# Kernel tuning notes

Hardware: AMD Instinct MI355X
Metric: run time of the kernel (lower is better)

The kernel has to match this reference:

```python
import jax, jax.numpy as jnp
import numpy as np

B, CIN, L = 4, 128, 2048
D_MODEL, D_STATE, EXPAND, HEADDIM, NGROUPS = 256, 16, 3, 3, 1
D_INNER = EXPAND * D_MODEL            # 768
NHEADS = D_INNER // HEADDIM           # 256
CONV_DIM = D_INNER + 2 * NGROUPS * D_STATE   # 800
D_IN_PROJ = 2 * D_INNER + 2 * NGROUPS * D_STATE + NHEADS  # 1824
K_PROJ, D_CONV = 4, 4
EPS = 1e-5


def setup_inputs() -> dict:
    key = jax.random.key(0)
    ks = jax.random.split(key, 9)
    x = jax.random.normal(ks[0], (B, CIN, L), jnp.float32)
    proj_w = jax.random.normal(ks[1], (D_MODEL, CIN, K_PROJ), jnp.float32) / np.float32(np.sqrt(CIN * K_PROJ))
    in_proj_w = jax.random.normal(ks[2], (D_IN_PROJ, D_MODEL), jnp.float32) / np.float32(np.sqrt(D_MODEL))
    conv_w = jax.random.normal(ks[3], (CONV_DIM, 1, D_CONV), jnp.float32) / np.float32(np.sqrt(D_CONV))
    conv_b = jax.random.normal(ks[4], (CONV_DIM,), jnp.float32) * 0.01
    # dt_bias = inverse-softplus of dt ~ LogUniform[1e-3, 1e-1] (mamba2 init)
    u = jax.random.uniform(ks[5], (NHEADS,), jnp.float32)
    dt = jnp.exp(u * np.float32(np.log(0.1) - np.log(1e-3)) + np.float32(np.log(1e-3)))
    dt_bias = dt + jnp.log(-jnp.expm1(-dt))
    A_log = jnp.log(1.0 + 15.0 * jax.random.uniform(ks[6], (NHEADS,), jnp.float32))  # A in [-16,-1]
    D_skip = jnp.ones((NHEADS,), jnp.float32)
    norm_w = jnp.ones((D_INNER,), jnp.float32)
    out_proj_w = jax.random.normal(ks[7], (D_MODEL, D_INNER), jnp.float32) / np.float32(np.sqrt(D_INNER))
    return {"x": x, "proj_w": proj_w, "in_proj_w": in_proj_w, "conv_w": conv_w,
            "conv_b": conv_b, "dt_bias": dt_bias, "A_log": A_log, "D_skip": D_skip,
            "norm_w": norm_w, "out_proj_w": out_proj_w}


def _forward(x, proj_w, in_proj_w, conv_w, conv_b, dt_bias, A_log, D_skip, norm_w, out_proj_w):
    # outer Conv1d, padding='same' (k=4 -> left 1, right 2), no bias: (B,CIN,L)->(B,D_MODEL,L)
    h = jax.lax.conv_general_dilated(x, proj_w, (1,), [(1, 2)],
                                     dimension_numbers=("NCH", "OIH", "NCH"))
    u = h.transpose(0, 2, 1)                          # (B, L, d_model)
    zxbcdt = jnp.einsum("bld,ed->ble", u, in_proj_w)  # (B, L, 1824)
    z = zxbcdt[..., :D_INNER]                                     # (B,L,768)
    xBC = zxbcdt[..., D_INNER:D_INNER + CONV_DIM]                 # (B,L,800)
    dt = zxbcdt[..., D_INNER + CONV_DIM:]                         # (B,L,256)
    dt = jax.nn.softplus(dt + dt_bias)
    # depthwise causal conv (pad d_conv-1 on left) + SiLU
    xBC_c = jax.lax.conv_general_dilated(xBC.transpose(0, 2, 1), conv_w, (1,), [(D_CONV - 1, 0)],
                                         feature_group_count=CONV_DIM,
                                         dimension_numbers=("NCH", "OIH", "NCH"))
    xBC = jax.nn.silu(xBC_c + conv_b[None, :, None]).transpose(0, 2, 1)  # (B,L,800)
    xs = xBC[..., :D_INNER].reshape(B, L, NHEADS, HEADDIM)        # (B,L,H,P)
    Bm = xBC[..., D_INNER:D_INNER + D_STATE]                      # (B,L,N) (ngroups=1)
    Cm = xBC[..., D_INNER + D_STATE:]                             # (B,L,N)
    A = -jnp.exp(A_log)                                           # (H,)

    def step(hst, inp):
        dt_t, x_t, B_t, C_t = inp                 # (B,H),(B,H,P),(B,N),(B,N)
        dA = jnp.exp(dt_t * A)[:, :, None, None]  # (B,H,1,1)
        hst = dA * hst + jnp.einsum("bh,bhp,bn->bhpn", dt_t, x_t, B_t)
        y_t = jnp.einsum("bhpn,bn->bhp", hst, C_t)
        return hst, y_t

    h0 = jnp.zeros((B, NHEADS, HEADDIM, D_STATE), x.dtype)
    _, ys = jax.lax.scan(step, h0, (dt.transpose(1, 0, 2), xs.transpose(1, 0, 2, 3),
                                    Bm.transpose(1, 0, 2), Cm.transpose(1, 0, 2)))
    y = ys.transpose(1, 0, 2, 3) + D_skip[None, None, :, None] * xs   # (B,L,H,P)
    y = y.reshape(B, L, D_INNER)
    # gated RMSNorm: gate first, then normalize (norm_before_gate=False)
    y = y * jax.nn.silu(z)
    y = y * jax.lax.rsqrt(jnp.mean(y * y, axis=-1, keepdims=True) + EPS) * norm_w
    out = jnp.einsum("ble,de->bld", y, out_proj_w)   # (B,L,d_model)
    return out.transpose(0, 2, 1)                    # (B,d_model,L)


def reference(x, proj_w, in_proj_w, conv_w, conv_b, dt_bias, A_log, D_skip, norm_w, out_proj_w):
    return _forward(x, proj_w, in_proj_w, conv_w, conv_b, dt_bias, A_log, D_skip, norm_w, out_proj_w)
```

## Files before the change

kernel.cpp:

```cpp
#include <hip/hip_runtime.h>
#include <hip/hip_fp16.h>
#include <math.h>

#define B_     4
#define CIN    128
#define LEN    2048
#define DMODEL 256
#define DSTATE 16
#define NHEADS 256
#define DINNER 768
#define CONVDIM 800
#define DINPROJ 1824
#define EPS_   1e-5f
#define CHUNK  64
#define NCHUNK 32

typedef _Float16 f16x8 __attribute__((ext_vector_type(8)));
typedef float    f32x4 __attribute__((ext_vector_type(4)));

__device__ __forceinline__ float silu_(float x){ return x / (1.0f + __expf(-x)); }
__device__ __forceinline__ float softplus_(float x){
    return x > 0.f ? x + log1pf(__expf(-x)) : log1pf(__expf(x));
}

__device__ __forceinline__ void gl2lds16(const _Float16* g, _Float16* l){
    __builtin_amdgcn_global_load_lds(
        (const __attribute__((address_space(1))) void*)g,
        (__attribute__((address_space(3))) void*)l, 16, 0, 0);
}

__global__ __launch_bounds__(256) void k_f2h(const float* __restrict__ a,
                                             _Float16* __restrict__ o, int n){
    for (int i = blockIdx.x * 256 + threadIdx.x; i < n; i += gridDim.x * 256)
        o[i] = (_Float16)a[i];
}

__global__ __launch_bounds__(256) void k_im2col(const float* __restrict__ x,
                                                _Float16* __restrict__ xcol){
    __shared__ float xs[CIN][68];
    int blk = blockIdx.x;
    int b  = blk >> 5;
    int l0 = (blk & 31) << 6;
    const float* xb = x + (size_t)b * CIN * LEN;
    for (int idx = threadIdx.x; idx < CIN * 67; idx += 256){
        int ci = idx / 67, j = idx % 67;
        int gl = l0 - 1 + j;
        xs[ci][j] = (gl >= 0 && gl < LEN) ? xb[ci * LEN + gl] : 0.f;
    }
    __syncthreads();
    #pragma unroll
    for (int v = 0; v < 16; v++){
        int id = v * 256 + threadIdx.x;
        int rl = id >> 6, c = id & 63;
        f16x8 pk;
        #pragma unroll
        for (int e = 0; e < 8; e++){
            int ci = c * 2 + (e >> 2), k = e & 3;
            pk[e] = (_Float16)xs[ci][rl + k];
        }
        *(f16x8*)&xcol[((size_t)(b * LEN + l0 + rl)) * 512 + c * 8] = pk;
    }
}

template<int K, int EPI>
__global__ __launch_bounds__(256) void k_gemm(const _Float16* __restrict__ A,
                                              const _Float16* __restrict__ Bw,
                                              const float* __restrict__ dt_bias,
                                              _Float16* __restrict__ o_u,
                                              _Float16* __restrict__ o_z,
                                              _Float16* __restrict__ o_xbc,
                                              _Float16* __restrict__ o_dt,
                                              float* __restrict__ o_f){
    __shared__ __align__(16) _Float16 As[128 * 32];
    __shared__ __align__(16) _Float16 Bs[128 * 32];
    int tid  = threadIdx.x;
    int wv   = tid >> 6;
    int lane = tid & 63;
    int quad = lane >> 4;
    int l16  = lane & 15;
    int m0 = blockIdx.x * 128;
    int n0 = blockIdx.y * 128;
    int wm = (wv >> 1) * 64;
    int wn = (wv & 1) * 64;
    int srow = lane >> 2;
    int scol = (lane & 3) * 8;

    f32x4 acc[4][4];
    #pragma unroll
    for (int i = 0; i < 4; i++)
        #pragma unroll
        for (int j = 0; j < 4; j++)
            acc[i][j] = (f32x4){0.f, 0.f, 0.f, 0.f};

    for (int k0 = 0; k0 < K; k0 += 32){
        #pragma unroll
        for (int j = 0; j < 2; j++){
            int ar = m0 + wv * 32 + j * 16 + srow;
            gl2lds16(A + (size_t)ar * K + k0 + scol,
                     &As[(wv * 32 + j * 16) * 32]);
            int nr = n0 + wv * 32 + j * 16 + srow;
            if (EPI == 1) nr = nr > (DINPROJ - 1) ? (DINPROJ - 1) : nr;
            gl2lds16(Bw + (size_t)nr * K + k0 + scol,
                     &Bs[(wv * 32 + j * 16) * 32]);
        }
        __syncthreads();
        f16x8 af[4], bf[4];
        #pragma unroll
        for (int i = 0; i < 4; i++)
            af[i] = *(const f16x8*)&As[(wm + i * 16 + l16) * 32 + quad * 8];
        #pragma unroll
        for (int j = 0; j < 4; j++)
            bf[j] = *(const f16x8*)&Bs[(wn + j * 16 + l16) * 32 + quad * 8];
        #pragma unroll
        for (int i = 0; i < 4; i++)
            #pragma unroll
            for (int j = 0; j < 4; j++)
                acc[i][j] = __builtin_amdgcn_mfma_f32_16x16x32_f16(
                                af[i], bf[j], acc[i][j], 0, 0, 0);
        __syncthreads();
    }

    if (EPI == 0){
        #pragma unroll
        for (int j = 0; j < 4; j++){
            int col = n0 + wn + j * 16 + l16;
            #pragma unroll
            for (int i = 0; i < 4; i++){
                int row = m0 + wm + i * 16 + quad * 4;
                #pragma unroll
                for (int r = 0; r < 4; r++)
                    o_u[(size_t)(row + r) * DMODEL + col] = (_Float16)acc[i][j][r];
            }
        }
    } else if (EPI == 1){
        #pragma unroll
        for (int j = 0; j < 4; j++){
            int col = n0 + wn + j * 16 + l16;
            if (col < DINNER){
                #pragma unroll
                for (int i = 0; i < 4; i++){
                    int row = m0 + wm + i * 16 + quad * 4;
                    #pragma unroll
                    for (int r = 0; r < 4; r++)
                        o_z[(size_t)(row + r) * DINNER + col] = (_Float16)acc[i][j][r];
                }
            } else if (col < DINNER + CONVDIM){
                int cc = col - DINNER;
                #pragma unroll
                for (int i = 0; i < 4; i++){
                    int row = m0 + wm + i * 16 + quad * 4;
                    #pragma unroll
                    for (int r = 0; r < 4; r++)
                        o_xbc[(size_t)(row + r) * CONVDIM + cc] = (_Float16)acc[i][j][r];
                }
            } else if (col < DINPROJ){
                int hh = col - (DINNER + CONVDIM);
                float bias = dt_bias[hh];
                #pragma unroll
                for (int i = 0; i < 4; i++){
                    int row = m0 + wm + i * 16 + quad * 4;
                    #pragma unroll
                    for (int r = 0; r < 4; r++)
                        o_dt[(size_t)(row + r) * NHEADS + hh] =
                            (_Float16)softplus_(acc[i][j][r] + bias);
                }
            }
        }
    } else {
        #pragma unroll
        for (int i = 0; i < 4; i++){
            int row = m0 + wm + i * 16 + quad * 4;
            int b = row >> 11, l = row & (LEN - 1);
            #pragma unroll
            for (int j = 0; j < 4; j++){
                int d = n0 + wn + j * 16 + l16;
                *(f32x4*)&o_f[(((size_t)(b * DMODEL + d)) << 11) + l] = acc[i][j];
            }
        }
    }
}

__global__ __launch_bounds__(256) void k_dwconv(const __half* __restrict__ xbc,
                                                const float* __restrict__ cw,
                                                const float* __restrict__ cb,
                                                __half* __restrict__ xcc){
    int idx = blockIdx.x * 256 + threadIdx.x;
    int c = idx % CONVDIM;
    int r = idx / CONVDIM;
    int l = r & (LEN - 1);
    float4 wv = *(const float4*)(cw + c * 4);
    float acc = cb[c];
    if (l >= 3){
        const __half* base = xbc + (size_t)(r - 3) * CONVDIM + c;
        acc += __half2float(base[0]) * wv.x + __half2float(base[CONVDIM]) * wv.y +
               __half2float(base[2 * CONVDIM]) * wv.z + __half2float(base[3 * CONVDIM]) * wv.w;
    } else {
        const float wk[4] = {wv.x, wv.y, wv.z, wv.w};
        for (int k = 0; k < 4; k++){
            int t = l - 3 + k;
            if (t >= 0) acc += __half2float(xbc[(size_t)(r + k - 3) * CONVDIM + c]) * wk[k];
        }
    }
    xcc[idx] = __float2half(silu_(acc));
}

__global__ __launch_bounds__(64) void k_scanA(const __half* __restrict__ dtb,
                                              const __half* __restrict__ xcc,
                                              const float* __restrict__ A_log,
                                              __half* __restrict__ cstate,
                                              float* __restrict__ dsum){
    int blk = blockIdx.x;
    int c  = blk & (NCHUNK - 1);
    int hg = (blk >> 5) & 63;
    int b  = blk >> 11;
    int lane = threadIdx.x;
    int hl = lane >> 4;
    int n  = lane & 15;
    int h  = hg * 4 + hl;
    int c0 = h * 3;
    float A = -__expf(A_log[h]);
    int t0 = c * CHUNK;
    const __half* xr  = xcc + ((size_t)b * LEN + t0) * CONVDIM;
    const __half* dtp = dtb + ((size_t)b * LEN + t0) * NHEADS + h;
    float h0 = 0.f, h1 = 0.f, h2 = 0.f, sdt = 0.f;
    for (int t = 0; t < CHUNK; t++){
        float vx0 = __half2float(xr[c0]);
        float vx1 = __half2float(xr[c0 + 1]);
        float vx2 = __half2float(xr[c0 + 2]);
        float vB  = __half2float(xr[DINNER + n]);
        float cdt = __half2float(dtp[(size_t)t * NHEADS]);
        float dA  = __expf(cdt * A);
        float dtB = cdt * vB;
        h0 = fmaf(h0, dA, vx0 * dtB);
        h1 = fmaf(h1, dA, vx1 * dtB);
        h2 = fmaf(h2, dA, vx2 * dtB);
        sdt += cdt;
        xr += CONVDIM;
    }
    size_t sbase = (((size_t)(b * NHEADS + h)) * NCHUNK + c) * 48;
    cstate[sbase + n]      = __float2half(h0);
    cstate[sbase + 16 + n] = __float2half(h1);
    cstate[sbase + 32 + n] = __float2half(h2);
    if (n == 0) dsum[(size_t)(b * NHEADS + h) * NCHUNK + c] = __expf(A * sdt);
}

__global__ __launch_bounds__(64) void k_scanB(__half* __restrict__ cstate,
                                              const float* __restrict__ dsum){
    int bh = blockIdx.x;
    int lane = threadIdx.x;
    if (lane >= 48) return;
    __half* st = cstate + (size_t)bh * NCHUNK * 48 + lane;
    const float* dd = dsum + (size_t)bh * NCHUNK;
    float H = 0.f;
    for (int c = 0; c < NCHUNK; c++){
        float d = dd[c];
        float s = __half2float(st[(size_t)c * 48]);
        st[(size_t)c * 48] = __float2half(H);
        H = fmaf(H, d, s);
    }
}

__global__ __launch_bounds__(64) void k_scanC(const __half* __restrict__ dtb,
                                              const __half* __restrict__ xcc,
                                              const float* __restrict__ A_log,
                                              const float* __restrict__ D_skip,
                                              const __half* __restrict__ cstate,
                                              __half* __restrict__ y){
    int blk = blockIdx.x;
    int c  = blk & (NCHUNK - 1);
    int hg = (blk >> 5) & 63;
    int b  = blk >> 11;
    int lane = threadIdx.x;
    int hl = lane >> 4;
    int n  = lane & 15;
    int h  = hg * 4 + hl;
    int c0 = h * 3;
    float A   = -__expf(A_log[h]);
    float Dsk = D_skip[h];
    int t0 = c * CHUNK;
    const __half* xr  = xcc + ((size_t)b * LEN + t0) * CONVDIM;
    const __half* dtp = dtb + ((size_t)b * LEN + t0) * NHEADS + h;
    size_t sbase = (((size_t)(b * NHEADS + h)) * NCHUNK + c) * 48;
    float h0 = __half2float(cstate[sbase + n]);
    float h1 = __half2float(cstate[sbase + 16 + n]);
    float h2 = __half2float(cstate[sbase + 32 + n]);
    __half* yp = y + ((size_t)b * LEN + t0) * DINNER + c0;
    for (int t = 0; t < CHUNK; t++){
        float vx0 = __half2float(xr[c0]);
        float vx1 = __half2float(xr[c0 + 1]);
        float vx2 = __half2float(xr[c0 + 2]);
        float vB  = __half2float(xr[DINNER + n]);
        float vC  = __half2float(xr[DINNER + DSTATE + n]);
        float cdt = __half2float(dtp[(size_t)t * NHEADS]);
        float dA  = __expf(cdt * A);
        float dtB = cdt * vB;
        h0 = fmaf(h0, dA, vx0 * dtB);
        h1 = fmaf(h1, dA, vx1 * dtB);
        h2 = fmaf(h2, dA, vx2 * dtB);
        float p0 = h0 * vC, p1 = h1 * vC, p2 = h2 * vC;
        #pragma unroll
        for (int m = 1; m < 16; m <<= 1){
            p0 += __shfl_xor(p0, m, 64);
            p1 += __shfl_xor(p1, m, 64);
            p2 += __shfl_xor(p2, m, 64);
        }
        if (n < 3){
            float pv = (n == 0) ? p0 : ((n == 1) ? p1 : p2);
            float xv = (n == 0) ? vx0 : ((n == 1) ? vx1 : vx2);
            yp[n] = __float2half(fmaf(Dsk, xv, pv));
        }
        xr += CONVDIM;
        yp += DINNER;
    }
}

__global__ __launch_bounds__(256) void k_norm(__half* __restrict__ y,
                                              const __half* __restrict__ z,
                                              const float* __restrict__ nw){
    __shared__ float wsum[4];
    size_t r = blockIdx.x;
    int tid = threadIdx.x;
    const __half* zr = z + r * DINNER;
    __half* yr = y + r * DINNER;
    int e0 = tid, e1 = tid + 256, e2 = tid + 512;
    float t0 = __half2float(yr[e0]) * silu_(__half2float(zr[e0]));
    float t1 = __half2float(yr[e1]) * silu_(__half2float(zr[e1]));
    float t2 = __half2float(yr[e2]) * silu_(__half2float(zr[e2]));
    float ss = t0 * t0 + t1 * t1 + t2 * t2;
    #pragma unroll
    for (int m = 1; m < 64; m <<= 1) ss += __shfl_xor(ss, m, 64);
    if ((tid & 63) == 0) wsum[tid >> 6] = ss;
    __syncthreads();
    float tot = wsum[0] + wsum[1] + wsum[2] + wsum[3];
    float sc = rsqrtf(tot / (float)DINNER + EPS_);
    yr[e0] = __float2half(t0 * sc * nw[e0]);
    yr[e1] = __float2half(t1 * sc * nw[e1]);
    yr[e2] = __float2half(t2 * sc * nw[e2]);
}

extern "C" void kernel_launch(void* const* d_in, const int* in_sizes, int n_in,
                              void* d_out, int out_size, void* d_ws, size_t ws_size,
                              hipStream_t stream) {
    const float* x          = (const float*)d_in[0];
    const float* proj_w     = (const float*)d_in[1];
    const float* in_proj_w  = (const float*)d_in[2];
    const float* conv_w     = (const float*)d_in[3];
    const float* conv_b     = (const float*)d_in[4];
    const float* dt_bias    = (const float*)d_in[5];
    const float* A_log      = (const float*)d_in[6];
    const float* D_skip     = (const float*)d_in[7];
    const float* norm_w     = (const float*)d_in[8];
    const float* out_proj_w = (const float*)d_in[9];
    float* out = (float*)d_out;

    char* ob = (char*)d_out;
    _Float16* pw_h  = (_Float16*)ob;
    _Float16* ipw_h = (_Float16*)(ob + 262144);

    char* wsb = (char*)d_ws;
    _Float16* xcol  = (_Float16*)(wsb);
    _Float16* u_h   = (_Float16*)(wsb + 8388608);
    __half*   xcc_h = (__half*)(wsb);
    __half*   z_h   = (__half*)(wsb + 13107200);
    __half*   xbc_h = (__half*)(wsb + 25690112);
    __half*   y_h   = xbc_h;
    __half*   dt_h  = (__half*)(wsb + 38797312);
    __half*   cstate= (__half*)(wsb + 42991616);
    float*    dsum  = (float*)(wsb + 46137344);
    _Float16* opw_h = (_Float16*)(wsb + 46268416);

    k_f2h   <<<64, 256, 0, stream>>>(proj_w,     pw_h,  DMODEL * CIN * 4);
    k_f2h   <<<64, 256, 0, stream>>>(in_proj_w,  ipw_h, DINPROJ * DMODEL);
    k_f2h   <<<64, 256, 0, stream>>>(out_proj_w, opw_h, DMODEL * DINNER);
    k_im2col<<<128, 256, 0, stream>>>(x, xcol);
    k_gemm<512, 0><<<dim3(64, 2), 256, 0, stream>>>(xcol, pw_h, nullptr,
        u_h, nullptr, nullptr, nullptr, nullptr);
    k_gemm<256, 1><<<dim3(64, 15), 256, 0, stream>>>(u_h, ipw_h, dt_bias,
        nullptr, (_Float16*)z_h, (_Float16*)xbc_h, (_Float16*)dt_h, nullptr);
    k_dwconv<<<25600, 256, 0, stream>>>(xbc_h, conv_w, conv_b, xcc_h);
    k_scanA <<<8192, 64, 0, stream>>>(dt_h, xcc_h, A_log, cstate, dsum);
    k_scanB <<<1024, 64, 0, stream>>>(cstate, dsum);
    k_scanC <<<8192, 64, 0, stream>>>(dt_h, xcc_h, A_log, D_skip, cstate, y_h);
    k_norm  <<<8192, 256, 0, stream>>>(y_h, z_h, norm_w);
    k_gemm<768, 2><<<dim3(64, 2), 256, 0, stream>>>((const _Float16*)y_h, opw_h,
        nullptr, nullptr, nullptr, nullptr, nullptr, out);
}
```

Baseline: 318.5 us.

## Restructure chunked scan: fuse intra-chunk pass, add parallel inter-chunk state fixup

The chunked selective scan used to make two sequential passes over every chunk: one pass produced the end-of-chunk states, then a second pass recomputed the recurrence from the carried-in state. Now a single pass computes the zero-initialised intra-chunk outputs and chunk states together. A new parallel fixup kernel then adds the carried state's contribution to y, using a prefix sum of dt for the decay and a dot product of C with the state. Separately, the three weight-conversion launches are merged into one kernel. The cost is an extra read-modify-write of y in fp16 plus a wave-level prefix scan, and fp16 rounding of the partial y may change accuracy slightly.

```diff
diff --git a/kernel.cpp b/kernel.cpp
--- a/kernel.cpp
+++ b/kernel.cpp
@@ -29,10 +29,19 @@
         (__attribute__((address_space(3))) void*)l, 16, 0, 0);
 }
 
-__global__ __launch_bounds__(256) void k_f2h(const float* __restrict__ a,
-                                             _Float16* __restrict__ o, int n){
-    for (int i = blockIdx.x * 256 + threadIdx.x; i < n; i += gridDim.x * 256)
-        o[i] = (_Float16)a[i];
+__global__ __launch_bounds__(256) void k_f2h3(const float* __restrict__ a0,
+                                              const float* __restrict__ a1,
+                                              const float* __restrict__ a2,
+                                              _Float16* __restrict__ o0,
+                                              _Float16* __restrict__ o1,
+                                              _Float16* __restrict__ o2,
+                                              int n0, int n1, int n2){
+    int total = n0 + n1 + n2;
+    for (int i = blockIdx.x * 256 + threadIdx.x; i < total; i += gridDim.x * 256){
+        if (i < n0)            o0[i] = (_Float16)a0[i];
+        else if (i < n0 + n1)  o1[i - n0] = (_Float16)a1[i - n0];
+        else                   o2[i - n0 - n1] = (_Float16)a2[i - n0 - n1];
+    }
 }
 
 __global__ __launch_bounds__(256) void k_im2col(const float* __restrict__ x,
@@ -204,68 +213,13 @@
     xcc[idx] = __float2half(silu_(acc));
 }
 
-__global__ __launch_bounds__(64) void k_scanA(const __half* __restrict__ dtb,
-                                              const __half* __restrict__ xcc,
-                                              const float* __restrict__ A_log,
-                                              __half* __restrict__ cstate,
-                                              float* __restrict__ dsum){
-    int blk = blockIdx.x;
-    int c  = blk & (NCHUNK - 1);
-    int hg = (blk >> 5) & 63;
-    int b  = blk >> 11;
-    int lane = threadIdx.x;
-    int hl = lane >> 4;
-    int n  = lane & 15;
-    int h  = hg * 4 + hl;
-    int c0 = h * 3;
-    float A = -__expf(A_log[h]);
-    int t0 = c * CHUNK;
-    const __half* xr  = xcc + ((size_t)b * LEN + t0) * CONVDIM;
-    const __half* dtp = dtb + ((size_t)b * LEN + t0) * NHEADS + h;
-    float h0 = 0.f, h1 = 0.f, h2 = 0.f, sdt = 0.f;
-    for (int t = 0; t < CHUNK; t++){
-        float vx0 = __half2float(xr[c0]);
-        float vx1 = __half2float(xr[c0 + 1]);
-        float vx2 = __half2float(xr[c0 + 2]);
-        float vB  = __half2float(xr[DINNER + n]);
-        float cdt = __half2float(dtp[(size_t)t * NHEADS]);
-        float dA  = __expf(cdt * A);
-        float dtB = cdt * vB;
-        h0 = fmaf(h0, dA, vx0 * dtB);
-        h1 = fmaf(h1, dA, vx1 * dtB);
-        h2 = fmaf(h2, dA, vx2 * dtB);
-        sdt += cdt;
-        xr += CONVDIM;
-    }
-    size_t sbase = (((size_t)(b * NHEADS + h)) * NCHUNK + c) * 48;
-    cstate[sbase + n]      = __float2half(h0);
-    cstate[sbase + 16 + n] = __float2half(h1);
-    cstate[sbase + 32 + n] = __float2half(h2);
-    if (n == 0) dsum[(size_t)(b * NHEADS + h) * NCHUNK + c] = __expf(A * sdt);
-}
-
-__global__ __launch_bounds__(64) void k_scanB(__half* __restrict__ cstate,
-                                              const float* __restrict__ dsum){
-    int bh = blockIdx.x;
-    int lane = threadIdx.x;
-    if (lane >= 48) return;
-    __half* st = cstate + (size_t)bh * NCHUNK * 48 + lane;
-    const float* dd = dsum + (size_t)bh * NCHUNK;
-    float H = 0.f;
-    for (int c = 0; c < NCHUNK; c++){
-        float d = dd[c];
-        float s = __half2float(st[(size_t)c * 48]);
-        st[(size_t)c * 48] = __float2half(H);
-        H = fmaf(H, d, s);
-    }
-}
-
-__global__ __launch_bounds__(64) void k_scanC(const __half* __restrict__ dtb,
-                                              const __half* __restrict__ xcc,
-                                              const float* __restrict__ A_log,
-                                              const float* __restrict__ D_skip,
-                                              const __half* __restrict__ cstate,
-                                              __half* __restrict__ y){
+__global__ __launch_bounds__(64) void k_scanAC(const __half* __restrict__ dtb,
+                                               const __half* __restrict__ xcc,
+                                               const float* __restrict__ A_log,
+                                               const float* __restrict__ D_skip,
+                                               __half* __restrict__ y,
+                                               __half* __restrict__ cstate,
+                                               float* __restrict__ dsum){
     int blk = blockIdx.x;
     int c  = blk & (NCHUNK - 1);
     int hg = (blk >> 5) & 63;
@@ -280,10 +234,7 @@
     int t0 = c * CHUNK;
     const __half* xr  = xcc + ((size_t)b * LEN + t0) * CONVDIM;
     const __half* dtp = dtb + ((size_t)b * LEN + t0) * NHEADS + h;
-    size_t sbase = (((size_t)(b * NHEADS + h)) * NCHUNK + c) * 48;
-    float h0 = __half2float(cstate[sbase + n]);
-    float h1 = __half2float(cstate[sbase + 16 + n]);
-    float h2 = __half2float(cstate[sbase + 32 + n]);
+    float h0 = 0.f, h1 = 0.f, h2 = 0.f, sdt = 0.f;
     __half* yp = y + ((size_t)b * LEN + t0) * DINNER + c0;
     for (int t = 0; t < CHUNK; t++){
         float vx0 = __half2float(xr[c0]);
@@ -297,6 +248,7 @@
         h0 = fmaf(h0, dA, vx0 * dtB);
         h1 = fmaf(h1, dA, vx1 * dtB);
         h2 = fmaf(h2, dA, vx2 * dtB);
+        sdt += cdt;
         float p0 = h0 * vC, p1 = h1 * vC, p2 = h2 * vC;
         #pragma unroll
         for (int m = 1; m < 16; m <<= 1){
@@ -312,6 +264,67 @@
         xr += CONVDIM;
         yp += DINNER;
     }
+    size_t sbase = (((size_t)(b * NHEADS + h)) * NCHUNK + c) * 48;
+    cstate[sbase + n]      = __float2half(h0);
+    cstate[sbase + 16 + n] = __float2half(h1);
+    cstate[sbase + 32 + n] = __float2half(h2);
+    if (n == 0) dsum[(size_t)(b * NHEADS + h) * NCHUNK + c] = __expf(A * sdt);
+}
+
+__global__ __launch_bounds__(64) void k_scanB(__half* __restrict__ cstate,
+                                              const float* __restrict__ dsum){
+    int bh = blockIdx.x;
+    int lane = threadIdx.x;
+    if (lane >= 48) return;
+    __half* st = cstate + (size_t)bh * NCHUNK * 48 + lane;
+    const float* dd = dsum + (size_t)bh * NCHUNK;
+    float H = 0.f;
+    for (int c = 0; c < NCHUNK; c++){
+        float d = dd[c];
+        float s = __half2float(st[(size_t)c * 48]);
+        st[(size_t)c * 48] = __float2half(H);
+        H = fmaf(H, d, s);
+    }
+}
+
+__global__ __launch_bounds__(256) void k_fixup(const __half* __restrict__ dtb,
+                                               const __half* __restrict__ xcc,
+                                               const float* __restrict__ A_log,
+                                               const __half* __restrict__ cstate,
+                                               __half* __restrict__ y){
+    int task = blockIdx.x * 4 + (threadIdx.x >> 6);
+    int lane = threadIdx.x & 63;
+    int c = task & (NCHUNK - 1);
+    int h = (task >> 5) & (NHEADS - 1);
+    int b = task >> 13;
+    float A = -__expf(A_log[h]);
+    size_t row = (size_t)b * LEN + c * CHUNK + lane;
+    float cum = __half2float(dtb[row * NHEADS + h]);
+    #pragma unroll
+    for (int m = 1; m < 64; m <<= 1){
+        float v = __shfl(cum, lane - m, 64);
+        if (lane >= m) cum += v;
+    }
+    float decay = __expf(A * cum);
+    const _Float16* cp = (const _Float16*)(xcc) + row * CONVDIM + DINNER + DSTATE;
+    f16x8 cv0 = *(const f16x8*)cp;
+    f16x8 cv1 = *(const f16x8*)(cp + 8);
+    const _Float16* hp = (const _Float16*)(cstate) + (size_t)task * 48;
+    f16x8 hv[6];
+    #pragma unroll
+    for (int i = 0; i < 6; i++) hv[i] = *(const f16x8*)(hp + i * 8);
+    float s0 = 0.f, s1 = 0.f, s2 = 0.f;
+    #pragma unroll
+    for (int e = 0; e < 8; e++){
+        float cl = (float)cv0[e], ch = (float)cv1[e];
+        s0 = fmaf(cl, (float)hv[0][e], s0); s0 = fmaf(ch, (float)hv[1][e], s0);
+        s1 = fmaf(cl, (float)hv[2][e], s1); s1 = fmaf(ch, (float)hv[3][e], s1);
+        s2 = fmaf(cl, (float)hv[4][e], s2); s2 = fmaf(ch, (float)hv[5][e], s2);
+    }
+    __half* yp = y + row * DINNER + h * 3;
+    yp[0] = __float2half(__half2float(yp[0]) + decay * s0);
+    yp[1] = __float2half(__half2float(yp[1]) + decay * s1);
+    yp[2] = __float2half(__half2float(yp[2]) + decay * s2);
 }
 
 __global__ __launch_bounds__(256) void k_norm(__half* __restrict__ y,
@@ -369,18 +382,19 @@
     float*    dsum  = (float*)(wsb + 46137344);
     _Float16* opw_h = (_Float16*)(wsb + 46268416);
 
-    k_f2h   <<<64, 256, 0, stream>>>(proj_w,     pw_h,  DMODEL * CIN * 4);
-    k_f2h   <<<64, 256, 0, stream>>>(in_proj_w,  ipw_h, DINPROJ * DMODEL);
-    k_f2h   <<<64, 256, 0, stream>>>(out_proj_w, opw_h, DMODEL * DINNER);
+    k_f2h3  <<<96, 256, 0, stream>>>(proj_w, in_proj_w, out_proj_w,
+                                     pw_h, ipw_h, opw_h,
+                                     DMODEL * CIN * 4, DINPROJ * DMODEL,
+                                     DMODEL * DINNER);
     k_im2col<<<128, 256, 0, stream>>>(x, xcol);
     k_gemm<512, 0><<<dim3(64, 2), 256, 0, stream>>>(xcol, pw_h, nullptr,
         u_h, nullptr, nullptr, nullptr, nullptr);
     k_gemm<256, 1><<<dim3(64, 15), 256, 0, stream>>>(u_h, ipw_h, dt_bias,
         nullptr, (_Float16*)z_h, (_Float16*)xbc_h, (_Float16*)dt_h, nullptr);
     k_dwconv<<<25600, 256, 0, stream>>>(xbc_h, conv_w, conv_b, xcc_h);
-    k_scanA <<<8192, 64, 0, stream>>>(dt_h, xcc_h, A_log, cstate, dsum);
+    k_scanAC<<<8192, 64, 0, stream>>>(dt_h, xcc_h, A_log, D_skip, y_h, cstate, dsum);
     k_scanB <<<1024, 64, 0, stream>>>(cstate, dsum);
-    k_scanC <<<8192, 64, 0, stream>>>(dt_h, xcc_h, A_log, D_skip, cstate, y_h);
+    k_fixup <<<8192, 256, 0, stream>>>(dt_h, xcc_h, A_log, cstate, y_h);
     k_norm  <<<8192, 256, 0, stream>>>(y_h, z_h, norm_w);
     k_gemm<768, 2><<<dim3(64, 2), 256, 0, stream>>>((const _Float16*)y_h, opw_h,
         nullptr, nullptr, nullptr, nullptr, nullptr, out);
```

Result: slower. 338.0 us (+6.1%).
